# Optimization experiments

Hardware: AMD Instinct MI355X
Metric: run time of the kernel (lower is better)

The kernel has to match this reference:

```python
import jax, jax.numpy as jnp
import numpy as np

N = 10000      # nodes of this type
T = 160000     # total metapath instances (ragged rows)
D = 256        # input_dim
P = 256        # pre_embed_dim
H = 512        # mlp_settings['layer_list'][0]
S = 64         # select_dim


def setup_inputs() -> dict:
    key = jax.random.key(0)
    ks = jax.random.split(key, 16)
    def w(k, shape):
        return jax.random.normal(k, shape, jnp.float32) / np.sqrt(shape[0]).astype(np.float32)
    return {
        "feat_A": jax.random.normal(ks[0], (N, D), jnp.float32),
        "feat_AP": jax.random.normal(ks[1], (T, D), jnp.float32),
        "feat_APA": jax.random.normal(ks[2], (T, 2 * D), jnp.float32),
        "seg_AP": jnp.sort(jax.random.randint(ks[3], (T,), 0, N, jnp.int32)),
        "seg_APA": jnp.sort(jax.random.randint(ks[4], (T,), 0, N, jnp.int32)),
        "type_weight": w(ks[5], (D, P)),
        "W_enc_AP": w(ks[6], (D, H)),   "b_enc_AP": jnp.zeros((H,), jnp.float32),
        "W_dec_AP": w(ks[7], (H, P)),   "b_dec_AP": jnp.zeros((P,), jnp.float32),
        "W_enc_APA": w(ks[8], (2 * D, H)), "b_enc_APA": jnp.zeros((H,), jnp.float32),
        "W_dec_APA": w(ks[9], (H, P)),  "b_dec_APA": jnp.zeros((P,), jnp.float32),
        "W_attn1": w(ks[10], (2 * P, 2 * P)),
        "W_attn2": w(ks[11], (2 * P, 1)),
        "W_cls": w(ks[12], (P, S)), "b_cls": jnp.zeros((S,), jnp.float32),
    }


def reference(feat_A, feat_AP, feat_APA, seg_AP, seg_APA, type_weight,
              W_enc_AP, b_enc_AP, W_dec_AP, b_dec_AP,
              W_enc_APA, b_enc_APA, W_dec_APA, b_dec_APA,
              W_attn1, W_attn2, W_cls, b_cls):
    # center node embedding (metapath of length 1): feat @ type_weight
    center = feat_A @ type_weight                                  # [N, P]

    def metapath_path(feat, seg, We, be, Wd, bd):
        # per-metapath MLP encode (Linear+ReLU) / decode (Linear)
        h = jax.nn.relu(feat @ We + be)                            # [T, H]
        dec = h @ Wd + bd                                          # [T, P]
        # ragged split + per-node sum aggregation; empty segments -> zeros
        return jax.ops.segment_sum(dec, seg, num_segments=N,
                                   indices_are_sorted=True)        # [N, P]

    inj_AP = metapath_path(feat_AP, seg_AP, W_enc_AP, b_enc_AP, W_dec_AP, b_dec_AP)
    inj_APA = metapath_path(feat_APA, seg_APA, W_enc_APA, b_enc_APA, W_dec_APA, b_dec_APA)

    def attn_score(inj):
        # attn = Tanh -> Linear(2P,2P,no bias) -> Linear(2P,1,no bias) -> LeakyReLU(0.1), then mean
        x = jnp.tanh(jnp.concatenate([center, inj], axis=1))       # [N, 2P]
        s = (x @ W_attn1) @ W_attn2                                # [N, 1]
        return jax.nn.leaky_relu(s, 0.1).mean()

    # index 0 corresponds to the length-1 metapath (never scored; fixed to 0)
    scores = jnp.stack([jnp.zeros((), jnp.float32), attn_score(inj_AP), attn_score(inj_APA)])
    wts = jax.nn.softmax(scores)                                   # [3]

    inj_AP = inj_AP * wts[1]
    inj_APA = inj_APA * wts[2]
    embed = (inj_AP + inj_APA) * 0.5                               # stack(...,dim=2).mean(dim=2)
    pre_embed = jax.nn.log_softmax((center + embed) @ W_cls + b_cls, axis=1)  # [N, S]
    return pre_embed, inj_AP, inj_APA
```

## Files before the change

kernel.cpp:

```cpp
#include <hip/hip_runtime.h>
#include <stdint.h>

typedef __bf16 bf16x8 __attribute__((ext_vector_type(8)));
typedef __bf16 bf16x4 __attribute__((ext_vector_type(4)));
typedef float  f32x4  __attribute__((ext_vector_type(4)));

#define N_NODES 10000
#define T_ROWS  160000
#define HDIM    512
#define PDIM    256

__device__ __forceinline__ f32x4 mfma16(bf16x8 a, bf16x8 b, f32x4 c) {
    return __builtin_amdgcn_mfma_f32_16x16x32_bf16(a, b, c, 0, 0, 0);
}

__device__ __forceinline__ void pack_one(const float* __restrict__ W,
                                         __bf16* __restrict__ out,
                                         int K, int Nc, int ltid) {
    int lane = ltid & 63;
    int t = ltid >> 6;
    int KT = K >> 5;
    int kt = t % KT, nt = t / KT;
    int col = (nt << 4) + (lane & 15);
    int krow = (kt << 5) + ((lane >> 4) << 3);
    __bf16* dst = out + ((size_t)ltid << 3);
#pragma unroll
    for (int e = 0; e < 8; ++e)
        dst[e] = (__bf16)W[(size_t)(krow + e) * Nc + col];
}

__global__ void pack5_kernel(
    const float* __restrict__ tw,    __bf16* __restrict__ twP,
    const float* __restrict__ WeAP,  __bf16* __restrict__ WeAPp,
    const float* __restrict__ WdAP,  __bf16* __restrict__ WdAPp,
    const float* __restrict__ WeAPA, __bf16* __restrict__ WeAPAp,
    const float* __restrict__ WdAPA, __bf16* __restrict__ WdAPAp)
{
    int tid = blockIdx.x * 256 + threadIdx.x;
    if      (tid <  8192) pack_one(tw,    twP,    256, 256, tid);
    else if (tid < 24576) pack_one(WeAP,  WeAPp,  256, 512, tid - 8192);
    else if (tid < 40960) pack_one(WdAP,  WdAPp,  512, 256, tid - 24576);
    else if (tid < 73728) pack_one(WeAPA, WeAPAp, 512, 512, tid - 40960);
    else if (tid < 90112) pack_one(WdAPA, WdAPAp, 512, 256, tid - 73728);
}

template<int DIN>
__device__ __forceinline__ void path_body(
    const float* __restrict__ X,
    const __bf16* __restrict__ WeP, const float* __restrict__ be,
    const __bf16* __restrict__ WdP, const float* __restrict__ bd,
    const int* __restrict__ seg,
    float* __restrict__ inj,
    int tile, __bf16* buf, int* segs)
{
    constexpr int LDX = DIN + 8;
    constexpr int LDH = HDIM + 8;
    constexpr int LDP = 260;
    constexpr int KT1 = DIN / 32;
    const int tid = threadIdx.x;
    const int row0 = tile * 64;
    if (tid < 64) segs[tid] = seg[row0 + tid];

#pragma unroll 4
    for (int i = tid; i < 64 * (DIN / 4); i += 512) {
        int r = i / (DIN / 4), c4 = i % (DIN / 4);
        float4 f = ((const float4*)X)[(size_t)(row0 + r) * (DIN / 4) + c4];
        bf16x4 h;
        h[0] = (__bf16)f.x; h[1] = (__bf16)f.y; h[2] = (__bf16)f.z; h[3] = (__bf16)f.w;
        *(bf16x4*)&buf[r * LDX + c4 * 4] = h;
    }
    __syncthreads();

    const int wave = tid >> 6, lane = tid & 63;
    const int lr = lane & 15, lg = lane >> 4;

    f32x4 acc1[4][4] = {};
    {
        const __bf16* w1 = WeP + ((size_t)(wave * 4) * KT1) * 512 + lane * 8;
        bf16x8 bX[4], bY[4], a[4];
#pragma unroll
        for (int ct = 0; ct < 4; ++ct) bX[ct] = *(const bf16x8*)&w1[(size_t)(ct * KT1) * 512];
        for (int kt = 0; kt < KT1; kt += 2) {
#pragma unroll
            for (int ct = 0; ct < 4; ++ct)
                bY[ct] = *(const bf16x8*)&w1[(size_t)(ct * KT1 + kt + 1) * 512];
            int ko = kt * 32 + lg * 8;
#pragma unroll
            for (int rt = 0; rt < 4; ++rt)
                a[rt] = *(const bf16x8*)&buf[(rt * 16 + lr) * LDX + ko];
            __builtin_amdgcn_s_setprio(1);
#pragma unroll
            for (int ct = 0; ct < 4; ++ct)
#pragma unroll
                for (int rt = 0; rt < 4; ++rt)
                    acc1[rt][ct] = mfma16(a[rt], bX[ct], acc1[rt][ct]);
            __builtin_amdgcn_s_setprio(0);
            int kn = (kt + 2 < KT1) ? kt + 2 : 0;
#pragma unroll
            for (int ct = 0; ct < 4; ++ct)
                bX[ct] = *(const bf16x8*)&w1[(size_t)(ct * KT1 + kn) * 512];
            ko = (kt + 1) * 32 + lg * 8;
#pragma unroll
            for (int rt = 0; rt < 4; ++rt)
                a[rt] = *(const bf16x8*)&buf[(rt * 16 + lr) * LDX + ko];
            __builtin_amdgcn_s_setprio(1);
#pragma unroll
            for (int ct = 0; ct < 4; ++ct)
#pragma unroll
                for (int rt = 0; rt < 4; ++rt)
                    acc1[rt][ct] = mfma16(a[rt], bY[ct], acc1[rt][ct]);
            __builtin_amdgcn_s_setprio(0);
        }
    }
    __syncthreads();

#pragma unroll
    for (int ct = 0; ct < 4; ++ct) {
        int col = wave * 64 + ct * 16 + lr;
        float bias = be[col];
#pragma unroll
        for (int rt = 0; rt < 4; ++rt) {
            int rbase = rt * 16 + lg * 4;
#pragma unroll
            for (int j = 0; j < 4; ++j) {
                float vl = acc1[rt][ct][j] + bias;
                buf[(rbase + j) * LDH + col] = (__bf16)(vl > 0.f ? vl : 0.f);
            }
        }
    }
    __syncthreads();

    f32x4 acc2[4][2] = {};
    {
        const __bf16* w2 = WdP + ((size_t)(wave * 2) * 16) * 512 + lane * 8;
        bf16x8 bX2[2], bY2[2], aX[4], aY[4];
#pragma unroll
        for (int ct = 0; ct < 2; ++ct) bX2[ct] = *(const bf16x8*)&w2[(size_t)(ct * 16) * 512];
#pragma unroll
        for (int rt = 0; rt < 4; ++rt)
            aX[rt] = *(const bf16x8*)&buf[(rt * 16 + lr) * LDH + lg * 8];
        for (int kt = 0; kt < 16; kt += 2) {
#pragma unroll
            for (int ct = 0; ct < 2; ++ct)
                bY2[ct] = *(const bf16x8*)&w2[(size_t)(ct * 16 + kt + 1) * 512];
            int ko = (kt + 1) * 32 + lg * 8;
#pragma unroll
            for (int rt = 0; rt < 4; ++rt)
                aY[rt] = *(const bf16x8*)&buf[(rt * 16 + lr) * LDH + ko];
            __builtin_amdgcn_s_setprio(1);
#pragma unroll
            for (int ct = 0; ct < 2; ++ct)
#pragma unroll
                for (int rt = 0; rt < 4; ++rt)
                    acc2[rt][ct] = mfma16(aX[rt], bX2[ct], acc2[rt][ct]);
            __builtin_amdgcn_s_setprio(0);
            int kn = (kt + 2 < 16) ? kt + 2 : 0;
#pragma unroll
            for (int ct = 0; ct < 2; ++ct)
                bX2[ct] = *(const bf16x8*)&w2[(size_t)(ct * 16 + kn) * 512];
            ko = kn * 32 + lg * 8;
#pragma unroll
            for (int rt = 0; rt < 4; ++rt)
                aX[rt] = *(const bf16x8*)&buf[(rt * 16 + lr) * LDH + ko];
            __builtin_amdgcn_s_setprio(1);
#pragma unroll
            for (int ct = 0; ct < 2; ++ct)
#pragma unroll
                for (int rt = 0; rt < 4; ++rt)
                    acc2[rt][ct] = mfma16(aY[rt], bY2[ct], acc2[rt][ct]);
            __builtin_amdgcn_s_setprio(0);
        }
    }
    __syncthreads();

    float* decs = (float*)buf;
#pragma unroll
    for (int ct = 0; ct < 2; ++ct) {
        int col = wave * 32 + ct * 16 + lr;
        float bias = bd[col];
#pragma unroll
        for (int rt = 0; rt < 4; ++rt) {
            int rbase = rt * 16 + lg * 4;
#pragma unroll
            for (int j = 0; j < 4; ++j)
                decs[(rbase + j) * LDP + col] = acc2[rt][ct][j] + bias;
        }
    }
    __syncthreads();

    {
        const int c  = wave * 32 + (lane & 31);
        const int rs = (lane >> 5) * 32;
        float run = decs[rs * LDP + c];
        int cur = segs[rs];
        int runstart = rs;
#pragma unroll
        for (int r = rs + 1; r < rs + 32; ++r) {
            int s = segs[r];
            float v = decs[r * LDP + c];
            if (s == cur) run += v;
            else {
                if (runstart != rs) inj[(size_t)cur * PDIM + c] = run;
                else atomicAdd(&inj[(size_t)cur * PDIM + c], run);
                cur = s; run = v; runstart = r;
            }
        }
        atomicAdd(&inj[(size_t)cur * PDIM + c], run);
    }
}

__global__ __launch_bounds__(512, 4) void paths_kernel(
    const float* __restrict__ featAP,  const float* __restrict__ featAPA,
    const __bf16* __restrict__ WeAPp,  const float* __restrict__ beAP,
    const __bf16* __restrict__ WdAPp,  const float* __restrict__ bdAP,
    const __bf16* __restrict__ WeAPAp, const float* __restrict__ beAPA,
    const __bf16* __restrict__ WdAPAp, const float* __restrict__ bdAPA,
    const int* __restrict__ segAP, const int* __restrict__ segAPA,
    float* __restrict__ injAP, float* __restrict__ injAPA)
{
    __shared__ __bf16 buf[64 * (HDIM + 8)];
    __shared__ int segs[64];
    int bid = blockIdx.x;
    int tile = bid >> 1;
    if (bid & 1)
        path_body<512>(featAPA, WeAPAp, beAPA, WdAPAp, bdAPA, segAPA, injAPA,
                       tile, buf, segs);
    else
        path_body<256>(featAP, WeAPp, beAP, WdAPp, bdAP, segAP, injAP,
                       tile, buf, segs);
}

__global__ __launch_bounds__(512, 4) void center_kernel(
    const float* __restrict__ feat, const __bf16* __restrict__ twP,
    float* __restrict__ center)
{
    constexpr int LDX = 264;
    __shared__ __bf16 xs[64 * LDX];
    const int tid = threadIdx.x;
    const int row0 = blockIdx.x * 64;
#pragma unroll 4
    for (int i = tid; i < 64 * 64; i += 512) {
        int r = i / 64, c4 = i % 64;
        int row = row0 + r;
        float4 f = {0.f, 0.f, 0.f, 0.f};
        if (row < N_NODES) f = ((const float4*)feat)[(size_t)row * 64 + c4];
        bf16x4 h;
        h[0] = (__bf16)f.x; h[1] = (__bf16)f.y; h[2] = (__bf16)f.z; h[3] = (__bf16)f.w;
        *(bf16x4*)&xs[r * LDX + c4 * 4] = h;
    }
    __syncthreads();

    const int wave = tid >> 6, lane = tid & 63;
    const int lr = lane & 15, lg = lane >> 4;
    f32x4 acc[4][2] = {};
    const __bf16* w = twP + ((size_t)(wave * 2) * 8) * 512 + lane * 8;
    for (int kt = 0; kt < 8; ++kt) {
        int ko = kt * 32 + lg * 8;
        bf16x8 a[4];
#pragma unroll
        for (int rt = 0; rt < 4; ++rt)
            a[rt] = *(const bf16x8*)&xs[(rt * 16 + lr) * LDX + ko];
#pragma unroll
        for (int ct = 0; ct < 2; ++ct) {
            bf16x8 b = *(const bf16x8*)&w[(size_t)(ct * 8 + kt) * 512];
#pragma unroll
            for (int rt = 0; rt < 4; ++rt)
                acc[rt][ct] = mfma16(a[rt], b, acc[rt][ct]);
        }
    }
#pragma unroll
    for (int ct = 0; ct < 2; ++ct) {
        int col = wave * 32 + ct * 16 + lr;
#pragma unroll
        for (int rt = 0; rt < 4; ++rt) {
            int rbase = rt * 16 + lg * 4;
#pragma unroll
            for (int j = 0; j < 4; ++j) {
                int row = row0 + rbase + j;
                if (row < N_NODES) center[(size_t)row * 256 + col] = acc[rt][ct][j];
            }
        }
    }
}

__global__ void attn_v_kernel(const float* __restrict__ W1, const float* __restrict__ W2,
                              float* __restrict__ v) {
    int k = threadIdx.x;
    float s = 0.f;
    for (int j = 0; j < 512; ++j) s += W1[k * 512 + j] * W2[j];
    v[k] = s;
}

__global__ __launch_bounds__(256, 4) void score2_kernel(
    const float* __restrict__ center, const float* __restrict__ injAP,
    const float* __restrict__ injAPA, const float* __restrict__ v,
    float* __restrict__ sacc)
{
    const int w = threadIdx.x >> 6, lane = threadIdx.x & 63;
    float l1 = 0.f, l2 = 0.f;
    for (int row = blockIdx.x * 4 + w; row < N_NODES; row += gridDim.x * 4) {
        float x1 = 0.f, x2 = 0.f;
#pragma unroll
        for (int k = 0; k < 4; ++k) {
            int c = lane + k * 64;
            size_t off = (size_t)row * 256 + c;
            float tc = tanhf(center[off]) * v[c];
            float vi = v[256 + c];
            x1 += tc + tanhf(injAP[off]) * vi;
            x2 += tc + tanhf(injAPA[off]) * vi;
        }
#pragma unroll
        for (int o = 32; o > 0; o >>= 1) {
            x1 += __shfl_xor(x1, o);
            x2 += __shfl_xor(x2, o);
        }
        if (lane == 0) {
            l1 += (x1 > 0.f) ? x1 : 0.1f * x1;
            l2 += (x2 > 0.f) ? x2 : 0.1f * x2;
        }
    }
    if (lane == 0) {
        atomicAdd(&sacc[0], l1);
        atomicAdd(&sacc[1], l2);
    }
}

__global__ __launch_bounds__(256, 4) void final_kernel(
    const float* __restrict__ center, const float* __restrict__ injAP,
    const float* __restrict__ injAPA, const float* __restrict__ sacc,
    const float* __restrict__ Wcls, const float* __restrict__ bcls,
    float* __restrict__ out0, float* __restrict__ out1, float* __restrict__ out2)
{
    __shared__ float zs[4][256];
    float s1 = sacc[0] * (1.f / N_NODES), s2 = sacc[1] * (1.f / N_NODES);
    float m0 = fmaxf(0.f, fmaxf(s1, s2));
    float e0 = expf(0.f - m0), e1 = expf(s1 - m0), e2 = expf(s2 - m0);
    float inv = 1.f / (e0 + e1 + e2);
    const float w1 = e1 * inv, w2 = e2 * inv;

    const int row0 = blockIdx.x * 4;
    for (int idx = threadIdx.x; idx < 1024; idx += 256) {
        int r = idx >> 8, c = idx & 255;
        size_t off = (size_t)(row0 + r) * 256 + c;
        float a = injAP[off] * w1, b = injAPA[off] * w2;
        out1[off] = a; out2[off] = b;
        zs[r][c] = center[off] + 0.5f * (a + b);
    }
    __syncthreads();
    const int g = threadIdx.x >> 6, j = threadIdx.x & 63;
    float logit = bcls[j];
    for (int k = 0; k < 256; ++k) logit += zs[g][k] * Wcls[k * 64 + j];
    float m = logit;
#pragma unroll
    for (int o = 32; o > 0; o >>= 1) m = fmaxf(m, __shfl_xor(m, o));
    float e = expf(logit - m);
    float se = e;
#pragma unroll
    for (int o = 32; o > 0; o >>= 1) se += __shfl_xor(se, o);
    out0[(size_t)(row0 + g) * 64 + j] = (logit - m) - logf(se);
}

extern "C" void kernel_launch(void* const* d_in, const int* in_sizes, int n_in,
                              void* d_out, int out_size, void* d_ws, size_t ws_size,
                              hipStream_t stream)
{
    const float* feat_A   = (const float*)d_in[0];
    const float* feat_AP  = (const float*)d_in[1];
    const float* feat_APA = (const float*)d_in[2];
    const int*   seg_AP   = (const int*)d_in[3];
    const int*   seg_APA  = (const int*)d_in[4];
    const float* type_w   = (const float*)d_in[5];
    const float* We_AP    = (const float*)d_in[6];
    const float* be_AP    = (const float*)d_in[7];
    const float* Wd_AP    = (const float*)d_in[8];
    const float* bd_AP    = (const float*)d_in[9];
    const float* We_APA   = (const float*)d_in[10];
    const float* be_APA   = (const float*)d_in[11];
    const float* Wd_APA   = (const float*)d_in[12];
    const float* bd_APA   = (const float*)d_in[13];
    const float* W_attn1  = (const float*)d_in[14];
    const float* W_attn2  = (const float*)d_in[15];
    const float* W_cls    = (const float*)d_in[16];
    const float* b_cls    = (const float*)d_in[17];

    char* ws = (char*)d_ws;
    size_t o = 0;
    auto alloc = [&](size_t bytes) { char* p = ws + o; o += (bytes + 255) & ~size_t(255); return p; };
    float* center = (float*)alloc((size_t)N_NODES * 256 * 4);
    float* injAP  = (float*)alloc((size_t)N_NODES * 256 * 4);
    float* injAPA = (float*)alloc((size_t)N_NODES * 256 * 4);
    float* vbuf   = (float*)alloc(512 * 4);
    float* sacc   = (float*)alloc(256);
    __bf16* twP    = (__bf16*)alloc(256 * 256 * 2);
    __bf16* WeAPp  = (__bf16*)alloc(256 * 512 * 2);
    __bf16* WdAPp  = (__bf16*)alloc(512 * 256 * 2);
    __bf16* WeAPAp = (__bf16*)alloc(512 * 512 * 2);
    __bf16* WdAPAp = (__bf16*)alloc(512 * 256 * 2);

    hipMemsetAsync(injAP,  0, (size_t)N_NODES * 256 * 4, stream);
    hipMemsetAsync(injAPA, 0, (size_t)N_NODES * 256 * 4, stream);
    hipMemsetAsync(sacc,   0, 256, stream);

    pack5_kernel<<<352, 256, 0, stream>>>(type_w, twP, We_AP, WeAPp, Wd_AP, WdAPp,
                                          We_APA, WeAPAp, Wd_APA, WdAPAp);
    attn_v_kernel<<<1, 512, 0, stream>>>(W_attn1, W_attn2, vbuf);
    center_kernel<<<(N_NODES + 63) / 64, 512, 0, stream>>>(feat_A, twP, center);
    paths_kernel<<<2 * (T_ROWS / 64), 512, 0, stream>>>(
        feat_AP, feat_APA, WeAPp, be_AP, WdAPp, bd_AP,
        WeAPAp, be_APA, WdAPAp, bd_APA, seg_AP, seg_APA, injAP, injAPA);
    score2_kernel<<<256, 256, 0, stream>>>(center, injAP, injAPA, vbuf, sacc);

    float* out0 = (float*)d_out;
    float* out1 = out0 + (size_t)N_NODES * 64;
    float* out2 = out1 + (size_t)N_NODES * 256;
    final_kernel<<<N_NODES / 4, 256, 0, stream>>>(center, injAP, injAPA, sacc,
                                                  W_cls, b_cls, out0, out1, out2);
}
```

Baseline: 427.9 us.

## Fuse center GEMM into paths kernel, fold attn vector into pack kernel

The center projection tiles become extra leading blocks of the paths kernel, and the attention-vector reduction becomes extra threads of the weight-pack kernel. This removes two kernel launches and lets the center work overlap with the path GEMMs. The encoder MFMA operands are swapped so each lane holds four consecutive hidden columns, which allows a vectorized bias load and bf16x4 LDS stores in the ReLU epilogue. One barrier before the per-wave segment reduction is dropped, relying on each wave reading only the columns it wrote itself.

Result: no change. 422.9 us (-1.2%).

```diff
diff --git a/kernel.cpp b/kernel.cpp
--- a/kernel.cpp
+++ b/kernel.cpp
@@ -9,6 +9,7 @@
 #define T_ROWS  160000
 #define HDIM    512
 #define PDIM    256
+#define NCTILES 157
 
 __device__ __forceinline__ f32x4 mfma16(bf16x8 a, bf16x8 b, f32x4 c) {
     return __builtin_amdgcn_mfma_f32_16x16x32_bf16(a, b, c, 0, 0, 0);
@@ -29,19 +30,27 @@
         dst[e] = (__bf16)W[(size_t)(krow + e) * Nc + col];
 }
 
-__global__ void pack5_kernel(
+__global__ void pack6_kernel(
     const float* __restrict__ tw,    __bf16* __restrict__ twP,
     const float* __restrict__ WeAP,  __bf16* __restrict__ WeAPp,
     const float* __restrict__ WdAP,  __bf16* __restrict__ WdAPp,
     const float* __restrict__ WeAPA, __bf16* __restrict__ WeAPAp,
-    const float* __restrict__ WdAPA, __bf16* __restrict__ WdAPAp)
-{
-    int tid = blockIdx.x * 256 + threadIdx.x;
+    const float* __restrict__ WdAPA, __bf16* __restrict__ WdAPAp,
+    const float* __restrict__ W1, const float* __restrict__ W2,
+    float* __restrict__ vbuf)
+{
+    int tid = blockIdx.x * 512 + threadIdx.x;
     if      (tid <  8192) pack_one(tw,    twP,    256, 256, tid);
     else if (tid < 24576) pack_one(WeAP,  WeAPp,  256, 512, tid - 8192);
     else if (tid < 40960) pack_one(WdAP,  WdAPp,  512, 256, tid - 24576);
     else if (tid < 73728) pack_one(WeAPA, WeAPAp, 512, 512, tid - 40960);
     else if (tid < 90112) pack_one(WdAPA, WdAPAp, 512, 256, tid - 73728);
+    else if (tid < 90624) {
+        int k = tid - 90112;
+        float s = 0.f;
+        for (int j = 0; j < 512; ++j) s += W1[k * 512 + j] * W2[j];
+        vbuf[k] = s;
+    }
 }
 
 template<int DIN>
@@ -79,53 +88,55 @@
         const __bf16* w1 = WeP + ((size_t)(wave * 4) * KT1) * 512 + lane * 8;
         bf16x8 bX[4], bY[4], a[4];
 #pragma unroll
-        for (int ct = 0; ct < 4; ++ct) bX[ct] = *(const bf16x8*)&w1[(size_t)(ct * KT1) * 512];
+        for (int ht = 0; ht < 4; ++ht) bX[ht] = *(const bf16x8*)&w1[(size_t)(ht * KT1) * 512];
         for (int kt = 0; kt < KT1; kt += 2) {
 #pragma unroll
-            for (int ct = 0; ct < 4; ++ct)
-                bY[ct] = *(const bf16x8*)&w1[(size_t)(ct * KT1 + kt + 1) * 512];
+            for (int ht = 0; ht < 4; ++ht)
+                bY[ht] = *(const bf16x8*)&w1[(size_t)(ht * KT1 + kt + 1) * 512];
             int ko = kt * 32 + lg * 8;
 #pragma unroll
-            for (int rt = 0; rt < 4; ++rt)
-                a[rt] = *(const bf16x8*)&buf[(rt * 16 + lr) * LDX + ko];
+            for (int xt = 0; xt < 4; ++xt)
+                a[xt] = *(const bf16x8*)&buf[(xt * 16 + lr) * LDX + ko];
             __builtin_amdgcn_s_setprio(1);
 #pragma unroll
-            for (int ct = 0; ct < 4; ++ct)
-#pragma unroll
-                for (int rt = 0; rt < 4; ++rt)
-                    acc1[rt][ct] = mfma16(a[rt], bX[ct], acc1[rt][ct]);
+            for (int ht = 0; ht < 4; ++ht)
+#pragma unroll
+                for (int xt = 0; xt < 4; ++xt)
+                    acc1[ht][xt] = mfma16(bX[ht], a[xt], acc1[ht][xt]);
             __builtin_amdgcn_s_setprio(0);
             int kn = (kt + 2 < KT1) ? kt + 2 : 0;
 #pragma unroll
-            for (int ct = 0; ct < 4; ++ct)
-                bX[ct] = *(const bf16x8*)&w1[(size_t)(ct * KT1 + kn) * 512];
+            for (int ht = 0; ht < 4; ++ht)
+                bX[ht] = *(const bf16x8*)&w1[(size_t)(ht * KT1 + kn) * 512];
             ko = (kt + 1) * 32 + lg * 8;
 #pragma unroll
-            for (int rt = 0; rt < 4; ++rt)
-                a[rt] = *(const bf16x8*)&buf[(rt * 16 + lr) * LDX + ko];
+            for (int xt = 0; xt < 4; ++xt)
+                a[xt] = *(const bf16x8*)&buf[(xt * 16 + lr) * LDX + ko];
             __builtin_amdgcn_s_setprio(1);
 #pragma unroll
-            for (int ct = 0; ct < 4; ++ct)
-#pragma unroll
-                for (int rt = 0; rt < 4; ++rt)
-                    acc1[rt][ct] = mfma16(a[rt], bY[ct], acc1[rt][ct]);
+            for (int ht = 0; ht < 4; ++ht)
+#pragma unroll
+                for (int xt = 0; xt < 4; ++xt)
+                    acc1[ht][xt] = mfma16(bY[ht], a[xt], acc1[ht][xt]);
             __builtin_amdgcn_s_setprio(0);
         }
     }
     __syncthreads();
 
 #pragma unroll
-    for (int ct = 0; ct < 4; ++ct) {
-        int col = wave * 64 + ct * 16 + lr;
-        float bias = be[col];
-#pragma unroll
-        for (int rt = 0; rt < 4; ++rt) {
-            int rbase = rt * 16 + lg * 4;
+    for (int ht = 0; ht < 4; ++ht) {
+        int hcol0 = wave * 64 + ht * 16 + lg * 4;
+        f32x4 bias = *(const f32x4*)&be[hcol0];
+#pragma unroll
+        for (int xt = 0; xt < 4; ++xt) {
+            int xrow = xt * 16 + lr;
+            bf16x4 hv;
 #pragma unroll
             for (int j = 0; j < 4; ++j) {
-                float vl = acc1[rt][ct][j] + bias;
-                buf[(rbase + j) * LDH + col] = (__bf16)(vl > 0.f ? vl : 0.f);
+                float vl = acc1[ht][xt][j] + bias[j];
+                hv[j] = (__bf16)(vl > 0.f ? vl : 0.f);
             }
+            *(bf16x4*)&buf[xrow * LDH + hcol0] = hv;
         }
     }
     __syncthreads();
@@ -186,7 +197,6 @@
                 decs[(rbase + j) * LDP + col] = acc2[rt][ct][j] + bias;
         }
     }
-    __syncthreads();
 
     {
         const int c  = wave * 32 + (lane & 31);
@@ -209,35 +219,13 @@
     }
 }
 
-__global__ __launch_bounds__(512, 4) void paths_kernel(
-    const float* __restrict__ featAP,  const float* __restrict__ featAPA,
-    const __bf16* __restrict__ WeAPp,  const float* __restrict__ beAP,
-    const __bf16* __restrict__ WdAPp,  const float* __restrict__ bdAP,
-    const __bf16* __restrict__ WeAPAp, const float* __restrict__ beAPA,
-    const __bf16* __restrict__ WdAPAp, const float* __restrict__ bdAPA,
-    const int* __restrict__ segAP, const int* __restrict__ segAPA,
-    float* __restrict__ injAP, float* __restrict__ injAPA)
-{
-    __shared__ __bf16 buf[64 * (HDIM + 8)];
-    __shared__ int segs[64];
-    int bid = blockIdx.x;
-    int tile = bid >> 1;
-    if (bid & 1)
-        path_body<512>(featAPA, WeAPAp, beAPA, WdAPAp, bdAPA, segAPA, injAPA,
-                       tile, buf, segs);
-    else
-        path_body<256>(featAP, WeAPp, beAP, WdAPp, bdAP, segAP, injAP,
-                       tile, buf, segs);
-}
-
-__global__ __launch_bounds__(512, 4) void center_kernel(
+__device__ __forceinline__ void center_body(
     const float* __restrict__ feat, const __bf16* __restrict__ twP,
-    float* __restrict__ center)
+    float* __restrict__ center, int tile, __bf16* xs)
 {
     constexpr int LDX = 264;
-    __shared__ __bf16 xs[64 * LDX];
     const int tid = threadIdx.x;
-    const int row0 = blockIdx.x * 64;
+    const int row0 = tile * 64;
 #pragma unroll 4
     for (int i = tid; i < 64 * 64; i += 512) {
         int r = i / 64, c4 = i % 64;
@@ -283,12 +271,32 @@
     }
 }
 
-__global__ void attn_v_kernel(const float* __restrict__ W1, const float* __restrict__ W2,
-                              float* __restrict__ v) {
-    int k = threadIdx.x;
-    float s = 0.f;
-    for (int j = 0; j < 512; ++j) s += W1[k * 512 + j] * W2[j];
-    v[k] = s;
+__global__ __launch_bounds__(512, 4) void paths_kernel(
+    const float* __restrict__ featAP,  const float* __restrict__ featAPA,
+    const __bf16* __restrict__ WeAPp,  const float* __restrict__ beAP,
+    const __bf16* __restrict__ WdAPp,  const float* __restrict__ bdAP,
+    const __bf16* __restrict__ WeAPAp, const float* __restrict__ beAPA,
+    const __bf16* __restrict__ WdAPAp, const float* __restrict__ bdAPA,
+    const int* __restrict__ segAP, const int* __restrict__ segAPA,
+    float* __restrict__ injAP, float* __restrict__ injAPA,
+    const float* __restrict__ featA, const __bf16* __restrict__ twP,
+    float* __restrict__ center)
+{
+    __shared__ __bf16 buf[64 * (HDIM + 8)];
+    __shared__ int segs[64];
+    int bid = blockIdx.x;
+    if (bid < NCTILES) {
+        center_body(featA, twP, center, bid, buf);
+        return;
+    }
+    int p = bid - NCTILES;
+    int tile = p >> 1;
+    if (p & 1)
+        path_body<512>(featAPA, WeAPAp, beAPA, WdAPAp, bdAPA, segAPA, injAPA,
+                       tile, buf, segs);
+    else
+        path_body<256>(featAP, WeAPp, beAP, WdAPp, bdAP, segAP, injAP,
+                       tile, buf, segs);
 }
 
 __global__ __launch_bounds__(256, 4) void score2_kernel(
@@ -401,13 +409,13 @@
     hipMemsetAsync(injAPA, 0, (size_t)N_NODES * 256 * 4, stream);
     hipMemsetAsync(sacc,   0, 256, stream);
 
-    pack5_kernel<<<352, 256, 0, stream>>>(type_w, twP, We_AP, WeAPp, Wd_AP, WdAPp,
-                                          We_APA, WeAPAp, Wd_APA, WdAPAp);
-    attn_v_kernel<<<1, 512, 0, stream>>>(W_attn1, W_attn2, vbuf);
-    center_kernel<<<(N_NODES + 63) / 64, 512, 0, stream>>>(feat_A, twP, center);
-    paths_kernel<<<2 * (T_ROWS / 64), 512, 0, stream>>>(
+    pack6_kernel<<<177, 512, 0, stream>>>(type_w, twP, We_AP, WeAPp, Wd_AP, WdAPp,
+                                          We_APA, WeAPAp, Wd_APA, WdAPAp,
+                                          W_attn1, W_attn2, vbuf);
+    paths_kernel<<<NCTILES + 2 * (T_ROWS / 64), 512, 0, stream>>>(
         feat_AP, feat_APA, WeAPp, be_AP, WdAPp, bd_AP,
-        WeAPAp, be_APA, WdAPAp, bd_APA, seg_AP, seg_APA, injAP, injAPA);
+        WeAPAp, be_APA, WdAPAp, bd_APA, seg_AP, seg_APA, injAP, injAPA,
+        feat_A, twP, center);
     score2_kernel<<<256, 256, 0, stream>>>(center, injAP, injAPA, vbuf, sacc);
 
     float* out0 = (float*)d_out;
```
